# Performance work log

Measured on AMD Instinct MI355X. Metric: run time of the kernel, lower is better.

## Reference

```python
import jax, jax.numpy as jnp
import numpy as np

T, B = 100, 256
DIMS = [784, 1024, 256]
DT, TAU_M, TAU_S = 1e-3, 0.02, 0.005
ALPHA = 1.0 - DT / TAU_S   # 0.8  (synaptic current decay)
BETA = 1.0 - DT / TAU_M    # 0.95 (membrane decay)


def lif_forward(x, W):
    """EventProp LIF layer forward. x: [T,B,d1], W: [d2,d1].
    Matches SpikingLinear_ev.manual_forward: step i uses input[i-1]; step 0 is all zeros.
    Returns spikes [T,B,d2], pre-reset voltage V_spikes, current I."""
    Bsz, d2 = x.shape[1], W.shape[0]
    I0 = jnp.zeros((Bsz, d2), x.dtype)
    V0 = jnp.zeros((Bsz, d2), x.dtype)

    def step(carry, x_t):
        I_prev, V_prev = carry
        I = ALPHA * I_prev + x_t @ W.T
        V_pre = BETA * V_prev + (1.0 - BETA) * I
        s = (V_pre > 1.0).astype(x.dtype)
        V = (1.0 - s) * V_pre  # reset-to-zero on spike
        return (I, V), (s, V_pre, I)

    _, (s, V_pre, I) = jax.lax.scan(step, (I0, V0), x[:-1])
    pad = jnp.zeros((1, Bsz, d2), x.dtype)
    spikes = jnp.concatenate([pad, s], axis=0)
    V_spikes = jnp.concatenate([pad, V_pre], axis=0)
    I_full = jnp.concatenate([pad, I], axis=0)
    return spikes, V_spikes, I_full


def setup_inputs() -> dict:
    key = jax.random.key(0)
    k1, k2, k3 = jax.random.split(key, 3)
    x = (jax.random.uniform(k1, (T, B, DIMS[0])) < 0.05).astype(jnp.float32)
    # kaiming_normal_ on [d2,d1]: std = sqrt(2/fan_in), fan_in = d1
    W1 = jax.random.normal(k2, (DIMS[1], DIMS[0]), jnp.float32) * np.float32(np.sqrt(2.0 / DIMS[0]))
    W2 = jax.random.normal(k3, (DIMS[2], DIMS[1]), jnp.float32) * np.float32(np.sqrt(2.0 / DIMS[1]))
    return {"x": x, "W1": W1, "W2": W2}


def reference(x, W1, W2):
    s1, _, _ = lif_forward(x, W1)
    s2, _, _ = lif_forward(s1, W2)
    return s2
```

## Files before the change

kernel.cpp:

```cpp
#include <hip/hip_runtime.h>
#include <hip/hip_bf16.h>


#define ALPHA_F 0.8f
#define BETA_F 0.95f
#define ONE_MINUS_BETA_F 0.05f

__global__ __launch_bounds__(256) void transpose_nt(const float* __restrict__ W,
                                                    float* __restrict__ WT,
                                                    int N, int K) {
    __shared__ float tile[32][33];
    const int k0 = blockIdx.x * 32, n0 = blockIdx.y * 32;
    const int tx = threadIdx.x & 31, ty = threadIdx.x >> 5;
#pragma unroll
    for (int r = 0; r < 4; ++r) {
        int n = n0 + ty + r * 8, k = k0 + tx;
        if (n < N && k < K) tile[ty + r * 8][tx] = W[(size_t)n * K + k];
    }
    __syncthreads();
#pragma unroll
    for (int r = 0; r < 4; ++r) {
        int k = k0 + ty + r * 8, n = n0 + tx;
        if (k < K && n < N) WT[(size_t)k * N + n] = tile[tx][ty + r * 8];
    }
}

__global__ __launch_bounds__(256) void precompact(const float* __restrict__ x,
                                                  int* __restrict__ cnts,
                                                  int* __restrict__ lists) {
    const int r = blockIdx.x * 4 + (threadIdx.x >> 6);
    const int lane = threadIdx.x & 63;
    const int k0 = lane * 4;
    unsigned flags = 0;
    if (lane < 49) {
        float4 v = *(const float4*)(x + (size_t)r * 784 + k0);
        flags = (v.x != 0.0f ? 1u : 0u) | (v.y != 0.0f ? 2u : 0u) |
                (v.z != 0.0f ? 4u : 0u) | (v.w != 0.0f ? 8u : 0u);
    }
    const unsigned long long m0 = __ballot(flags & 1u);
    const unsigned long long m1 = __ballot(flags & 2u);
    const unsigned long long m2 = __ballot(flags & 4u);
    const unsigned long long m3 = __ballot(flags & 8u);
    const int c0 = __popcll(m0), c1 = __popcll(m1), c2 = __popcll(m2);
    const unsigned long long lm = ((unsigned long long)1 << lane) - 1;
    int* lrow = lists + (size_t)r * 160;
    if (flags & 1u) lrow[__popcll(m0 & lm)] = k0 + 0;
    if (flags & 2u) lrow[c0 + __popcll(m1 & lm)] = k0 + 1;
    if (flags & 4u) lrow[c0 + c1 + __popcll(m2 & lm)] = k0 + 2;
    if (flags & 8u) lrow[c0 + c1 + c2 + __popcll(m3 & lm)] = k0 + 3;
    if (lane == 0) cnts[r] = c0 + c1 + c2 + __popcll(m3);
}

__global__ __launch_bounds__(256) void sparse1(const int* __restrict__ cnts,
                                               const int* __restrict__ lists,
                                               const float* __restrict__ W1T,
                                               float* __restrict__ C1) {
    const int tid = threadIdx.x;
    const int row = blockIdx.x;
    const int n = cnts[row];
    const int* lst = lists + (size_t)row * 160;
    const float* wbase = W1T + tid * 4;
    float4 acc = {0.0f, 0.0f, 0.0f, 0.0f};
    int i = 0;
    for (; i + 8 <= n; i += 8) {
        float4 w0 = *(const float4*)(wbase + (size_t)lst[i + 0] * 1024);
        float4 w1 = *(const float4*)(wbase + (size_t)lst[i + 1] * 1024);
        float4 w2 = *(const float4*)(wbase + (size_t)lst[i + 2] * 1024);
        float4 w3 = *(const float4*)(wbase + (size_t)lst[i + 3] * 1024);
        float4 w4 = *(const float4*)(wbase + (size_t)lst[i + 4] * 1024);
        float4 w5 = *(const float4*)(wbase + (size_t)lst[i + 5] * 1024);
        float4 w6 = *(const float4*)(wbase + (size_t)lst[i + 6] * 1024);
        float4 w7 = *(const float4*)(wbase + (size_t)lst[i + 7] * 1024);
        acc.x += ((w0.x + w1.x) + (w2.x + w3.x)) + ((w4.x + w5.x) + (w6.x + w7.x));
        acc.y += ((w0.y + w1.y) + (w2.y + w3.y)) + ((w4.y + w5.y) + (w6.y + w7.y));
        acc.z += ((w0.z + w1.z) + (w2.z + w3.z)) + ((w4.z + w5.z) + (w6.z + w7.z));
        acc.w += ((w0.w + w1.w) + (w2.w + w3.w)) + ((w4.w + w5.w) + (w6.w + w7.w));
    }
    for (; i < n; ++i) {
        float4 w0 = *(const float4*)(wbase + (size_t)lst[i] * 1024);
        acc.x += w0.x; acc.y += w0.y; acc.z += w0.z; acc.w += w0.w;
    }
    *(float4*)(C1 + (size_t)row * 1024 + tid * 4) = acc;
}

__global__ __launch_bounds__(256) void scan1(const float* __restrict__ C1,
                                             unsigned long long* __restrict__ S1b) {
    const int idx = blockIdx.x * 256 + threadIdx.x;
    const int word = idx >> 6;
    const int lane = threadIdx.x & 63;
    if (lane == 0) S1b[word] = 0ull;
    float I = 0.0f, V = 0.0f;
#pragma unroll 7
    for (int t = 1; t <= 98; ++t) {
        float c = C1[(size_t)(t - 1) * 262144 + idx];
        I = ALPHA_F * I + c;
        float Vp = BETA_F * V + ONE_MINUS_BETA_F * I;
        const bool sp = Vp > 1.0f;
        unsigned long long m = __ballot(sp);
        V = sp ? 0.0f : Vp;
        if (lane == 0) S1b[(size_t)t * 4096 + word] = m;
    }
}

__global__ __launch_bounds__(256) void sparse2(const unsigned long long* __restrict__ S1b,
                                               const float* __restrict__ W2T,
                                               float* __restrict__ C2) {
    const int r = __builtin_amdgcn_readfirstlane(blockIdx.x * 4 + (threadIdx.x >> 6));
    const int lane = threadIdx.x & 63;
    const unsigned long long* mrow = S1b + (size_t)r * 16;
    float4 acc = {0, 0, 0, 0};
#pragma unroll 1
    for (int j = 0; j < 16; ++j) {
        unsigned long long m = mrow[j];
        while (m) {
            const int bit = __ffsll((long long)m) - 1;
            m &= m - 1;
            const int k = j * 64 + bit;
            float4 w = *(const float4*)(W2T + (size_t)k * 256 + lane * 4);
            acc.x += w.x; acc.y += w.y; acc.z += w.z; acc.w += w.w;
        }
    }
    *(float4*)(C2 + (size_t)r * 256 + lane * 4) = acc;
}

__global__ __launch_bounds__(256) void scan2(const float* __restrict__ C2,
                                             float* __restrict__ out) {
    const int idx = blockIdx.x * 256 + threadIdx.x;
    out[idx] = 0.0f;
    float I = 0.0f, V = 0.0f;
#pragma unroll 9
    for (int t = 1; t <= 99; ++t) {
        float c = C2[(size_t)(t - 1) * 65536 + idx];
        I = ALPHA_F * I + c;
        float Vp = BETA_F * V + ONE_MINUS_BETA_F * I;
        float s = (Vp > 1.0f) ? 1.0f : 0.0f;
        V = (1.0f - s) * Vp;
        out[(size_t)t * 65536 + idx] = s;
    }
}

extern "C" void kernel_launch(void* const* d_in, const int* in_sizes, int n_in,
                              void* d_out, int out_size, void* d_ws, size_t ws_size,
                              hipStream_t stream) {
    const float* x  = (const float*)d_in[0];
    const float* W1 = (const float*)d_in[1];
    const float* W2 = (const float*)d_in[2];
    float* out = (float*)d_out;

    char* ws = (char*)d_ws;
    float* C1 = (float*)ws;
    unsigned long long* S1b = (unsigned long long*)(ws + 102760448);
    float* W1T = (float*)(ws + 106004480);
    float* W2T = (float*)(ws + 109215744);
    int* cnts  = (int*)(ws + 110264320);
    int* lists = (int*)(ws + 110364672);
    float* C2 = C1;

    precompact<<<25088 / 4, 256, 0, stream>>>(x, cnts, lists);
    transpose_nt<<<dim3(25, 32), 256, 0, stream>>>(W1, W1T, 1024, 784);
    transpose_nt<<<dim3(32, 8), 256, 0, stream>>>(W2, W2T, 256, 1024);

    sparse1<<<25088, 256, 0, stream>>>(cnts, lists, W1T, C1);
    scan1<<<1024, 256, 0, stream>>>(C1, S1b);
    sparse2<<<25344 / 4, 256, 0, stream>>>(S1b, W2T, C2);
    scan2<<<256, 256, 0, stream>>>(C2, out);
}
```

Measured before the change: 224.7 us.

## Stage W1T column slices in LDS for the first-layer sparse gather

The layer-1 sparse accumulation kernel is restructured. Each block now loads a 784x16 column slice of the transposed weights into padded shared memory, then processes 256 input rows against it, with 16 threads per row each owning one output column. This replaces per-row float4 gathers of full 4 KB weight rows from global/L2 with reuse from LDS, cutting global gather traffic. In exchange it uses about 53 KB of LDS per block, which limits occupancy, adds possible bank conflicts on the index-driven LDS reads, and writes outputs in narrower 64-byte segments.

```diff
diff --git a/kernel.cpp b/kernel.cpp
--- a/kernel.cpp
+++ b/kernel.cpp
@@ -51,36 +51,53 @@
     if (lane == 0) cnts[r] = c0 + c1 + c2 + __popcll(m3);
 }
 
-__global__ __launch_bounds__(256) void sparse1(const int* __restrict__ cnts,
-                                               const int* __restrict__ lists,
-                                               const float* __restrict__ W1T,
-                                               float* __restrict__ C1) {
+__global__ __launch_bounds__(256) void sparse1_lds(const int* __restrict__ cnts,
+                                                   const int* __restrict__ lists,
+                                                   const float* __restrict__ W1T,
+                                                   float* __restrict__ C1) {
+    __shared__ float w[784 * 17];
+    const int ct = blockIdx.x;
+    const int chunk = blockIdx.y;
     const int tid = threadIdx.x;
-    const int row = blockIdx.x;
-    const int n = cnts[row];
-    const int* lst = lists + (size_t)row * 160;
-    const float* wbase = W1T + tid * 4;
-    float4 acc = {0.0f, 0.0f, 0.0f, 0.0f};
-    int i = 0;
-    for (; i + 8 <= n; i += 8) {
-        float4 w0 = *(const float4*)(wbase + (size_t)lst[i + 0] * 1024);
-        float4 w1 = *(const float4*)(wbase + (size_t)lst[i + 1] * 1024);
-        float4 w2 = *(const float4*)(wbase + (size_t)lst[i + 2] * 1024);
-        float4 w3 = *(const float4*)(wbase + (size_t)lst[i + 3] * 1024);
-        float4 w4 = *(const float4*)(wbase + (size_t)lst[i + 4] * 1024);
-        float4 w5 = *(const float4*)(wbase + (size_t)lst[i + 5] * 1024);
-        float4 w6 = *(const float4*)(wbase + (size_t)lst[i + 6] * 1024);
-        float4 w7 = *(const float4*)(wbase + (size_t)lst[i + 7] * 1024);
-        acc.x += ((w0.x + w1.x) + (w2.x + w3.x)) + ((w4.x + w5.x) + (w6.x + w7.x));
-        acc.y += ((w0.y + w1.y) + (w2.y + w3.y)) + ((w4.y + w5.y) + (w6.y + w7.y));
-        acc.z += ((w0.z + w1.z) + (w2.z + w3.z)) + ((w4.z + w5.z) + (w6.z + w7.z));
-        acc.w += ((w0.w + w1.w) + (w2.w + w3.w)) + ((w4.w + w5.w) + (w6.w + w7.w));
+
+    {
+        const int kl = tid >> 2;
+        const int cp = (tid & 3) * 4;
+        for (int p = 0; p < 13; ++p) {
+            const int k = p * 64 + kl;
+            if (k < 784) {
+                const float4 v = *(const float4*)(W1T + (size_t)k * 1024 + ct * 16 + cp);
+                float* dst = w + k * 17 + cp;
+                dst[0] = v.x; dst[1] = v.y; dst[2] = v.z; dst[3] = v.w;
+            }
+        }
     }
-    for (; i < n; ++i) {
-        float4 w0 = *(const float4*)(wbase + (size_t)lst[i] * 1024);
-        acc.x += w0.x; acc.y += w0.y; acc.z += w0.z; acc.w += w0.w;
+    __syncthreads();
+
+    const int gid = tid >> 4;
+    const int c = tid & 15;
+
+    for (int j = 0; j < 16; ++j) {
+        const int r = chunk * 256 + j * 16 + gid;
+        const int n = cnts[r];
+        const int* lst = lists + (size_t)r * 160;
+        float acc = 0.0f;
+        int i = 0;
+        int4 pa, pb;
+        if (n >= 8) { pa = *(const int4*)lst; pb = *(const int4*)(lst + 4); }
+        while (i + 8 <= n) {
+            const int4 ca = pa, cb = pb;
+            i += 8;
+            if (i + 8 <= n) { pa = *(const int4*)(lst + i); pb = *(const int4*)(lst + i + 4); }
+            const float a0 = w[ca.x * 17 + c], a1 = w[ca.y * 17 + c];
+            const float a2 = w[ca.z * 17 + c], a3 = w[ca.w * 17 + c];
+            const float a4 = w[cb.x * 17 + c], a5 = w[cb.y * 17 + c];
+            const float a6 = w[cb.z * 17 + c], a7 = w[cb.w * 17 + c];
+            acc += ((a0 + a1) + (a2 + a3)) + ((a4 + a5) + (a6 + a7));
+        }
+        for (; i < n; ++i) acc += w[lst[i] * 17 + c];
+        C1[(size_t)r * 1024 + ct * 16 + c] = acc;
     }
-    *(float4*)(C1 + (size_t)row * 1024 + tid * 4) = acc;
 }
 
 __global__ __launch_bounds__(256) void scan1(const float* __restrict__ C1,
@@ -160,7 +177,7 @@
     transpose_nt<<<dim3(25, 32), 256, 0, stream>>>(W1, W1T, 1024, 784);
     transpose_nt<<<dim3(32, 8), 256, 0, stream>>>(W2, W2T, 256, 1024);
 
-    sparse1<<<25088, 256, 0, stream>>>(cnts, lists, W1T, C1);
+    sparse1_lds<<<dim3(64, 98), 256, 0, stream>>>(cnts, lists, W1T, C1);
     scan1<<<1024, 256, 0, stream>>>(C1, S1b);
     sparse2<<<25344 / 4, 256, 0, stream>>>(S1b, W2T, C2);
     scan2<<<256, 256, 0, stream>>>(C2, out);
```

Result: slower. 447.2 us (+99.0%).

## Merge prep kernels into one launch and skip empty layer-2 rows

Applied to the files above, without the earlier changes.

Fuses the input compaction and both weight transposes into a single prep kernel, cutting two launches. sparse2 now records a per-row flag saying whether any layer-1 spike occurred and writes C2 only for non-empty rows. scan2 reads the flag and loads C2 only when the row has spikes, which saves memory traffic on silent timesteps. The cost is an extra byte read per step and a branch in scan2.

```diff
diff --git a/kernel.cpp b/kernel.cpp
--- a/kernel.cpp
+++ b/kernel.cpp
@@ -6,49 +6,62 @@
 #define BETA_F 0.95f
 #define ONE_MINUS_BETA_F 0.05f
 
-__global__ __launch_bounds__(256) void transpose_nt(const float* __restrict__ W,
-                                                    float* __restrict__ WT,
-                                                    int N, int K) {
+__global__ __launch_bounds__(256) void prep(const float* __restrict__ x,
+                                            const float* __restrict__ W1,
+                                            const float* __restrict__ W2,
+                                            float* __restrict__ W1T,
+                                            float* __restrict__ W2T,
+                                            int* __restrict__ cnts,
+                                            int* __restrict__ lists) {
     __shared__ float tile[32][33];
-    const int k0 = blockIdx.x * 32, n0 = blockIdx.y * 32;
-    const int tx = threadIdx.x & 31, ty = threadIdx.x >> 5;
+    const int bid = blockIdx.x;
+    const int tid = threadIdx.x;
+
+    if (bid < 6272) {
+        const int r = bid * 4 + (tid >> 6);
+        const int lane = tid & 63;
+        const int k0 = lane * 4;
+        unsigned flags = 0;
+        if (lane < 49) {
+            float4 v = *(const float4*)(x + (size_t)r * 784 + k0);
+            flags = (v.x != 0.0f ? 1u : 0u) | (v.y != 0.0f ? 2u : 0u) |
+                    (v.z != 0.0f ? 4u : 0u) | (v.w != 0.0f ? 8u : 0u);
+        }
+        const unsigned long long m0 = __ballot(flags & 1u);
+        const unsigned long long m1 = __ballot(flags & 2u);
+        const unsigned long long m2 = __ballot(flags & 4u);
+        const unsigned long long m3 = __ballot(flags & 8u);
+        const int c0 = __popcll(m0), c1 = __popcll(m1), c2 = __popcll(m2);
+        const unsigned long long lm = ((unsigned long long)1 << lane) - 1;
+        int* lrow = lists + (size_t)r * 160;
+        if (flags & 1u) lrow[__popcll(m0 & lm)] = k0 + 0;
+        if (flags & 2u) lrow[c0 + __popcll(m1 & lm)] = k0 + 1;
+        if (flags & 4u) lrow[c0 + c1 + __popcll(m2 & lm)] = k0 + 2;
+        if (flags & 8u) lrow[c0 + c1 + c2 + __popcll(m3 & lm)] = k0 + 3;
+        if (lane == 0) cnts[r] = c0 + c1 + c2 + __popcll(m3);
+    } else {
+        const float* W; float* WT; int N, K, tk, tn;
+        if (bid < 7072) {
+            W = W1; WT = W1T; N = 1024; K = 784;
+            const int i = bid - 6272; tk = i % 25; tn = i / 25;
+        } else {
+            W = W2; WT = W2T; N = 256; K = 1024;
+            const int i = bid - 7072; tk = i % 32; tn = i / 32;
+        }
+        const int k0 = tk * 32, n0 = tn * 32;
+        const int tx = tid & 31, ty = tid >> 5;
 #pragma unroll
-    for (int r = 0; r < 4; ++r) {
-        int n = n0 + ty + r * 8, k = k0 + tx;
-        if (n < N && k < K) tile[ty + r * 8][tx] = W[(size_t)n * K + k];
+        for (int r = 0; r < 4; ++r) {
+            int n = n0 + ty + r * 8, k = k0 + tx;
+            if (n < N && k < K) tile[ty + r * 8][tx] = W[(size_t)n * K + k];
+        }
+        __syncthreads();
+#pragma unroll
+        for (int r = 0; r < 4; ++r) {
+            int k = k0 + ty + r * 8, n = n0 + tx;
+            if (k < K && n < N) WT[(size_t)k * N + n] = tile[tx][ty + r * 8];
+        }
     }
-    __syncthreads();
-#pragma unroll
-    for (int r = 0; r < 4; ++r) {
-        int k = k0 + ty + r * 8, n = n0 + tx;
-        if (k < K && n < N) WT[(size_t)k * N + n] = tile[tx][ty + r * 8];
-    }
-}
-
-__global__ __launch_bounds__(256) void precompact(const float* __restrict__ x,
-                                                  int* __restrict__ cnts,
-                                                  int* __restrict__ lists) {
-    const int r = blockIdx.x * 4 + (threadIdx.x >> 6);
-    const int lane = threadIdx.x & 63;
-    const int k0 = lane * 4;
-    unsigned flags = 0;
-    if (lane < 49) {
-        float4 v = *(const float4*)(x + (size_t)r * 784 + k0);
-        flags = (v.x != 0.0f ? 1u : 0u) | (v.y != 0.0f ? 2u : 0u) |
-                (v.z != 0.0f ? 4u : 0u) | (v.w != 0.0f ? 8u : 0u);
-    }
-    const unsigned long long m0 = __ballot(flags & 1u);
-    const unsigned long long m1 = __ballot(flags & 2u);
-    const unsigned long long m2 = __ballot(flags & 4u);
-    const unsigned long long m3 = __ballot(flags & 8u);
-    const int c0 = __popcll(m0), c1 = __popcll(m1), c2 = __popcll(m2);
-    const unsigned long long lm = ((unsigned long long)1 << lane) - 1;
-    int* lrow = lists + (size_t)r * 160;
-    if (flags & 1u) lrow[__popcll(m0 & lm)] = k0 + 0;
-    if (flags & 2u) lrow[c0 + __popcll(m1 & lm)] = k0 + 1;
-    if (flags & 4u) lrow[c0 + c1 + __popcll(m2 & lm)] = k0 + 2;
-    if (flags & 8u) lrow[c0 + c1 + c2 + __popcll(m3 & lm)] = k0 + 3;
-    if (lane == 0) cnts[r] = c0 + c1 + c2 + __popcll(m3);
 }
 
 __global__ __launch_bounds__(256) void sparse1(const int* __restrict__ cnts,
@@ -104,14 +117,17 @@
 
 __global__ __launch_bounds__(256) void sparse2(const unsigned long long* __restrict__ S1b,
                                                const float* __restrict__ W2T,
-                                               float* __restrict__ C2) {
+                                               float* __restrict__ C2,
+                                               unsigned char* __restrict__ rowflag) {
     const int r = __builtin_amdgcn_readfirstlane(blockIdx.x * 4 + (threadIdx.x >> 6));
     const int lane = threadIdx.x & 63;
     const unsigned long long* mrow = S1b + (size_t)r * 16;
     float4 acc = {0, 0, 0, 0};
+    unsigned long long any = 0ull;
 #pragma unroll 1
     for (int j = 0; j < 16; ++j) {
         unsigned long long m = mrow[j];
+        any |= m;
         while (m) {
             const int bit = __ffsll((long long)m) - 1;
             m &= m - 1;
@@ -120,22 +136,27 @@
             acc.x += w.x; acc.y += w.y; acc.z += w.z; acc.w += w.w;
         }
     }
-    *(float4*)(C2 + (size_t)r * 256 + lane * 4) = acc;
+    if (lane == 0) rowflag[r] = any ? 1 : 0;
+    if (any) *(float4*)(C2 + (size_t)r * 256 + lane * 4) = acc;
 }
 
 __global__ __launch_bounds__(256) void scan2(const float* __restrict__ C2,
+                                             const unsigned char* __restrict__ rowflag,
                                              float* __restrict__ out) {
-    const int idx = blockIdx.x * 256 + threadIdx.x;
-    out[idx] = 0.0f;
+    const int b = blockIdx.x;
+    const int tid = threadIdx.x;
+    out[b * 256 + tid] = 0.0f;
     float I = 0.0f, V = 0.0f;
-#pragma unroll 9
+#pragma unroll 4
     for (int t = 1; t <= 99; ++t) {
-        float c = C2[(size_t)(t - 1) * 65536 + idx];
+        const int r = (t - 1) * 256 + b;
+        float c = 0.0f;
+        if (rowflag[r]) c = C2[(size_t)r * 256 + tid];
         I = ALPHA_F * I + c;
         float Vp = BETA_F * V + ONE_MINUS_BETA_F * I;
         float s = (Vp > 1.0f) ? 1.0f : 0.0f;
         V = (1.0f - s) * Vp;
-        out[(size_t)t * 65536 + idx] = s;
+        out[(size_t)t * 65536 + b * 256 + tid] = s;
     }
 }
 
@@ -154,14 +175,12 @@
     float* W2T = (float*)(ws + 109215744);
     int* cnts  = (int*)(ws + 110264320);
     int* lists = (int*)(ws + 110364672);
+    unsigned char* rowflag = (unsigned char*)(ws + 126420992);
     float* C2 = C1;
 
-    precompact<<<25088 / 4, 256, 0, stream>>>(x, cnts, lists);
-    transpose_nt<<<dim3(25, 32), 256, 0, stream>>>(W1, W1T, 1024, 784);
-    transpose_nt<<<dim3(32, 8), 256, 0, stream>>>(W2, W2T, 256, 1024);
-
+    prep<<<7328, 256, 0, stream>>>(x, W1, W2, W1T, W2T, cnts, lists);
     sparse1<<<25088, 256, 0, stream>>>(cnts, lists, W1T, C1);
     scan1<<<1024, 256, 0, stream>>>(C1, S1b);
-    sparse2<<<25344 / 4, 256, 0, stream>>>(S1b, W2T, C2);
-    scan2<<<256, 256, 0, stream>>>(C2, out);
+    sparse2<<<25344 / 4, 256, 0, stream>>>(S1b, W2T, C2, rowflag);
+    scan2<<<256, 256, 0, stream>>>(C2, rowflag, out);
 }
```

After: 240.9 us. +7.2%, slower.
